# Kernel tuning notes

Measured on AMD Instinct MI355X. Metric: run time of the kernel, lower is better.

Reference implementation:

```python
import jax, jax.numpy as jnp
import numpy as np

B, S, P = 2, 1024, 1024          # batch, new tokens, start_pos (cached prefix)
E, H, KV, HD = 2048, 32, 8, 64    # embed, heads, kv groups, head_dim
G = H // KV                       # group size = 4
THETA = 500000.0
CTX = P + S                       # cache/context length = 2048


def _rope_tables(start, seqlen):
    inv_freq = 1.0 / (THETA ** (jnp.arange(0, HD, 2, dtype=jnp.float32) / HD))
    pos = jnp.arange(start, start + seqlen, dtype=jnp.float32)
    freqs = jnp.outer(pos, inv_freq)              # [S, HD/2]
    emb = jnp.concatenate([freqs, freqs], axis=-1)  # [S, HD]
    return jnp.cos(emb), jnp.sin(emb)


def setup_inputs() -> dict:
    key = jax.random.key(0)
    ks = jax.random.split(key, 8)
    x = jax.random.normal(ks[0], (B, S, E), dtype=jnp.float32)
    cos1, sin1 = _rope_tables(P, S)
    cos = jnp.broadcast_to(cos1[None], (B, S, HD))
    sin = jnp.broadcast_to(sin1[None], (B, S, HD))
    # causal-with-offset additive mask: query i (global pos P+i) sees key j <= P+i
    qpos = P + jnp.arange(S)[:, None]
    kpos = jnp.arange(CTX)[None, :]
    mask = jnp.where(kpos <= qpos, 0.0, -1e9).astype(jnp.float32)[None, None]  # [1,1,S,CTX]
    cache_k = jax.random.normal(ks[1], (B, KV, CTX, HD), dtype=jnp.float32)
    cache_v = jax.random.normal(ks[2], (B, KV, CTX, HD), dtype=jnp.float32)
    sc = 0.02
    Wq = jax.random.normal(ks[3], (E, E), dtype=jnp.float32) * sc
    Wk = jax.random.normal(ks[4], (KV * HD, E), dtype=jnp.float32) * sc
    Wv = jax.random.normal(ks[5], (KV * HD, E), dtype=jnp.float32) * sc
    Wo = jax.random.normal(ks[6], (E, E), dtype=jnp.float32) * sc
    return {"x": x, "cos": cos, "sin": sin, "mask": mask,
            "cache_k": cache_k, "cache_v": cache_v,
            "Wq": Wq, "Wk": Wk, "Wv": Wv, "Wo": Wo, "start_pos": P}


def _rotate_half(t):
    t1, t2 = t[..., : HD // 2], t[..., HD // 2:]
    return jnp.concatenate([-t2, t1], axis=-1)


def _apply_rope(t, cos, sin):
    # t: [B, nh, S, HD]; cos/sin: [B, S, HD] -> unsqueeze head dim
    c = cos[:, None]
    s = sin[:, None]
    return t * c + _rotate_half(t) * s


def reference(x, cos, sin, mask, cache_k, cache_v, Wq, Wk, Wv, Wo, start_pos):
    b, s, e = x.shape
    q = (x @ Wq.T).reshape(b, s, H, HD).transpose(0, 2, 1, 3)    # [B,H,S,HD]
    k = (x @ Wk.T).reshape(b, s, KV, HD).transpose(0, 2, 1, 3)   # [B,KV,S,HD]
    v = (x @ Wv.T).reshape(b, s, KV, HD).transpose(0, 2, 1, 3)
    q = _apply_rope(q, cos, sin)
    k = _apply_rope(k, cos, sin)
    ck = cache_k.at[:, :, start_pos:start_pos + s].set(k)
    cv = cache_v.at[:, :, start_pos:start_pos + s].set(v)
    keys = ck[:, :, : start_pos + s]      # [B,KV,T,HD]
    vals = cv[:, :, : start_pos + s]
    # GQA without materializing repeated KV: view q as [B,KV,G,S,HD]
    qg = q.reshape(b, KV, G, s, HD)
    scores = jnp.einsum("bkgsh,bkth->bkgst", qg, keys) / jnp.sqrt(jnp.float32(HD))
    scores = scores + mask[:, :, None]    # broadcast mask over group dim
    probs = jax.nn.softmax(scores.astype(jnp.float32), axis=-1).astype(x.dtype)
    out = jnp.einsum("bkgst,bkth->bkgsh", probs, vals)            # [B,KV,G,S,HD]
    out = out.reshape(b, H, s, HD).transpose(0, 2, 1, 3).reshape(b, s, e)
    return out @ Wo.T
```

## Files before the change

### kernel.cpp

```cpp
#include <hip/hip_runtime.h>
#include <cstddef>

#define B   2
#define S   1024
#define PP  1024
#define CTX 2048
#define E   2048
#define H   32
#define KVH 8
#define HD  64
#define GQ  4
#define NQKV 3072

typedef short s4v  __attribute__((ext_vector_type(4)));
typedef short s8v  __attribute__((ext_vector_type(8)));
typedef float f4v  __attribute__((ext_vector_type(4)));

__device__ __forceinline__ short f2bf(float f) {
  union { float f; unsigned u; } v; v.f = f;
  unsigned r = v.u + 0x7fffu + ((v.u >> 16) & 1u);
  return (short)(r >> 16);
}
__device__ __forceinline__ float bf2f(short h) {
  union { unsigned u; float f; } v; v.u = ((unsigned)(unsigned short)h) << 16;
  return v.f;
}

__device__ __forceinline__ void gl_lds16(const void* g, void* l) {
  __builtin_amdgcn_global_load_lds((const __attribute__((address_space(1))) unsigned*)g,
                                   (__attribute__((address_space(3))) unsigned*)l, 16, 0, 0);
}

__global__ __launch_bounds__(256) void prep(const float* __restrict__ x,
                                            const float* __restrict__ Wq,
                                            const float* __restrict__ Wk,
                                            const float* __restrict__ Wv,
                                            short* __restrict__ xb,
                                            short* __restrict__ wqkv) {
  const int blk = blockIdx.x, tid = threadIdx.x;
  const float* s; short* d; int base;
  if (blk < 2048)      { s = x;  d = xb;             base = blk; }
  else if (blk < 4096) { s = Wq; d = wqkv;           base = blk - 2048; }
  else if (blk < 4608) { s = Wk; d = wqkv + 4194304; base = blk - 4096; }
  else                 { s = Wv; d = wqkv + 5242880; base = blk - 4608; }
  int i = (base * 256 + tid) * 8;
  float4 a = *(const float4*)&s[i];
  float4 b = *(const float4*)&s[i + 4];
  s8v o;
  o[0]=f2bf(a.x); o[1]=f2bf(a.y); o[2]=f2bf(a.z); o[3]=f2bf(a.w);
  o[4]=f2bf(b.x); o[5]=f2bf(b.y); o[6]=f2bf(b.z); o[7]=f2bf(b.w);
  *(s8v*)&d[i] = o;
}

__global__ __launch_bounds__(256) void qkv_gemm(const short* __restrict__ A,
                                                const short* __restrict__ Bw,
                                                const float* __restrict__ cosb,
                                                const float* __restrict__ sinb,
                                                const float* __restrict__ Wo,
                                                const float* __restrict__ ck,
                                                const float* __restrict__ cv,
                                                short* __restrict__ qb,
                                                short* __restrict__ keys,
                                                short* __restrict__ vt,
                                                short* __restrict__ wob) {
  __shared__ short As[2][8192];
  __shared__ short Bs[2][4096];
  const int tid = threadIdx.x;
  const int id  = blockIdx.x;

  if (id >= 768) {
    const int aux = id - 768;
    if (aux < 2048) {
      int i = (aux * 256 + tid) * 8;
      float4 a = *(const float4*)&Wo[i];
      float4 b = *(const float4*)&Wo[i + 4];
      s8v o;
      o[0]=f2bf(a.x); o[1]=f2bf(a.y); o[2]=f2bf(a.z); o[3]=f2bf(a.w);
      o[4]=f2bf(b.x); o[5]=f2bf(b.y); o[6]=f2bf(b.z); o[7]=f2bf(b.w);
      *(s8v*)&wob[i] = o;
    } else if (aux < 2560) {
      int idx = (aux - 2048) * 256 + tid;
      int bkv = idx >> 13;
      int rem = idx & 8191;
      size_t off = (size_t)bkv * (CTX * HD) + (size_t)rem * 8;
      float4 a = *(const float4*)&ck[off];
      float4 b = *(const float4*)&ck[off + 4];
      s8v o;
      o[0]=f2bf(a.x); o[1]=f2bf(a.y); o[2]=f2bf(a.z); o[3]=f2bf(a.w);
      o[4]=f2bf(b.x); o[5]=f2bf(b.y); o[6]=f2bf(b.z); o[7]=f2bf(b.w);
      *(s8v*)&keys[off] = o;
    } else {
      short (*Ts)[72] = (short (*)[72])&As[0][0];
      const int blk2 = aux - 2560;
      const int bkv = blk2 >> 4;
      const int p0  = (blk2 & 15) * 64;
      const float* src = cv + (size_t)bkv * CTX * HD + (size_t)p0 * HD;
      {
        int dq = tid & 15, kb = tid >> 4;
        float4 vv[4];
#pragma unroll
        for (int i = 0; i < 4; i++)
          vv[i] = *(const float4*)&src[(size_t)(kb * 4 + i) * HD + dq * 4];
#pragma unroll
        for (int j = 0; j < 4; j++) {
          s4v p;
          p[0]=f2bf(((const float*)&vv[0])[j]); p[1]=f2bf(((const float*)&vv[1])[j]);
          p[2]=f2bf(((const float*)&vv[2])[j]); p[3]=f2bf(((const float*)&vv[3])[j]);
          *(s4v*)&Ts[dq * 4 + j][kb * 4] = p;
        }
      }
      __syncthreads();
      {
        int d = tid >> 2, c = tid & 3;
        short* dst = vt + ((size_t)bkv * HD + d) * CTX + p0 + (c >> 1) * 32 + (c & 1) * 4;
#pragma unroll
        for (int j = 0; j < 4; j++) {
          s4v q4 = *(const s4v*)&Ts[d][c * 16 + j * 4];
          *(s4v*)&dst[j * 8] = q4;
        }
      }
    }
    return;
  }

  const int wv   = tid >> 6, lane = tid & 63;
  const int n16  = lane & 15, g = lane >> 4;
  const int m0   = (id / 48) * 128, n0 = (id % 48) * 64;
  const int K = 2048;

  const int rr = tid >> 3;
  const int cc = ((tid & 7) ^ (rr & 7)) * 8;
  const short* pA = A  + (size_t)(m0 + rr) * K + cc;
  const short* pB = Bw + (size_t)(n0 + rr) * K + cc;

  auto stage = [&](int buf, int kofs) {
#pragma unroll
    for (int st = 0; st < 4; st++)
      gl_lds16(pA + kofs + (size_t)st * 32 * K, &As[buf][(st * 256 + wv * 64) * 8]);
#pragma unroll
    for (int st = 0; st < 2; st++)
      gl_lds16(pB + kofs + (size_t)st * 32 * K, &Bs[buf][(st * 256 + wv * 64) * 8]);
  };

  f4v acc[2][4] = {};
  stage(0, 0);
  stage(1, 64);
  int cur = 0;
  for (int k0 = 0; k0 < K; k0 += 64) {
    if (k0 + 64 < K) asm volatile("s_waitcnt vmcnt(6)" ::: "memory");
    else             asm volatile("s_waitcnt vmcnt(0)" ::: "memory");
    __builtin_amdgcn_sched_barrier(0);
    __builtin_amdgcn_s_barrier();

#pragma unroll
    for (int kk = 0; kk < 2; kk++) {
      const int slot = (((kk << 2) | g) ^ (n16 & 7)) * 8;
      s8v af[2], bf[4];
#pragma unroll
      for (int mt = 0; mt < 2; mt++)
        af[mt] = *(const s8v*)&As[cur][(wv * 32 + mt * 16 + n16) * 64 + slot];
#pragma unroll
      for (int nt = 0; nt < 4; nt++)
        bf[nt] = *(const s8v*)&Bs[cur][(nt * 16 + n16) * 64 + slot];
#pragma unroll
      for (int mt = 0; mt < 2; mt++)
#pragma unroll
        for (int nt = 0; nt < 4; nt++)
          acc[mt][nt] = __builtin_amdgcn_mfma_f32_16x16x32_bf16(af[mt], bf[nt], acc[mt][nt], 0, 0, 0);
    }

    __builtin_amdgcn_s_barrier();
    if (k0 + 128 < K) stage(cur, k0 + 128);
    cur ^= 1;
  }

  const int rowb = m0 + wv * 32 + g * 4;
  if (n0 < 2048) {
#pragma unroll
    for (int mt = 0; mt < 2; mt++)
#pragma unroll
      for (int nt = 0; nt < 4; nt++) {
        size_t base = (size_t)(rowb + mt * 16) * E + n0 + nt * 16 + n16;
#pragma unroll
        for (int r = 0; r < 4; r++)
          qb[base + (size_t)r * E] = f2bf(acc[mt][nt][r]);
      }
  } else if (n0 < 2560) {
    const int kvh = (n0 - 2048) >> 6;
#pragma unroll
    for (int mt = 0; mt < 2; mt++) {
      const int row = rowb + mt * 16;
      const int bb = row >> 10, s = row & 1023;
      const float* crow = cosb + ((size_t)bb * S + s) * HD;
      const float* srow = sinb + ((size_t)bb * S + s) * HD;
      const size_t kdst = (((size_t)bb * KVH + kvh) * CTX + PP + s) * HD;
#pragma unroll
      for (int nt = 0; nt < 2; nt++) {
        const int d = n16 + nt * 16;
#pragma unroll
        for (int r = 0; r < 4; r++) {
          float c  = crow[r * HD + d];
          float sn = srow[r * HD + d];
          float k1 = acc[mt][nt][r], k2 = acc[mt][nt + 2][r];
          keys[kdst + (size_t)r * HD + d]      = f2bf(k1 * c - k2 * sn);
          keys[kdst + (size_t)r * HD + d + 32] = f2bf(k2 * c + k1 * sn);
        }
      }
    }
  } else {
    const int b    = m0 >> 10;
    const int head = (n0 - 2560) >> 6;
    const int sbase = (m0 - (b << 10)) + (wv >> 1) * 64;
    const size_t vrowb = (size_t)(b * KVH + head) * HD;
#pragma unroll
    for (int mt = 0; mt < 2; mt++) {
      const int mtp = (wv & 1) * 2 + mt;
      const int pos = PP + sbase + ((mtp >> 1) << 5) + ((mtp & 1) << 2) + (g << 3);
#pragma unroll
      for (int nt = 0; nt < 4; nt++) {
        const int d = nt * 16 + n16;
        s4v o;
        o[0] = f2bf(acc[mt][nt][0]); o[1] = f2bf(acc[mt][nt][1]);
        o[2] = f2bf(acc[mt][nt][2]); o[3] = f2bf(acc[mt][nt][3]);
        *(s4v*)&vt[(vrowb + d) * CTX + pos] = o;
      }
    }
  }
}

__global__ __launch_bounds__(256) void oproj_gemm(const short* __restrict__ A,
                                                  const short* __restrict__ Bw,
                                                  float* __restrict__ C) {
  __shared__ short As[2][8192];
  __shared__ short Bs[2][4096];
  const int tid  = threadIdx.x;
  const int wv   = tid >> 6, lane = tid & 63;
  const int n16  = lane & 15, g = lane >> 4;
  const int id   = blockIdx.x;
  const int m0   = (id >> 5) * 128, n0 = (id & 31) * 64;
  const int K = E, N = E;

  const int rr = tid >> 3;
  const int cc = ((tid & 7) ^ (rr & 7)) * 8;
  const short* pA = A  + (size_t)(m0 + rr) * K + cc;
  const short* pB = Bw + (size_t)(n0 + rr) * K + cc;

  auto stage = [&](int buf, int kofs) {
#pragma unroll
    for (int st = 0; st < 4; st++)
      gl_lds16(pA + kofs + (size_t)st * 32 * K, &As[buf][(st * 256 + wv * 64) * 8]);
#pragma unroll
    for (int st = 0; st < 2; st++)
      gl_lds16(pB + kofs + (size_t)st * 32 * K, &Bs[buf][(st * 256 + wv * 64) * 8]);
  };

  f4v acc[2][4] = {};
  stage(0, 0);
  stage(1, 64);
  int cur = 0;
  for (int k0 = 0; k0 < K; k0 += 64) {
    if (k0 + 64 < K) asm volatile("s_waitcnt vmcnt(6)" ::: "memory");
    else             asm volatile("s_waitcnt vmcnt(0)" ::: "memory");
    __builtin_amdgcn_sched_barrier(0);
    __builtin_amdgcn_s_barrier();

#pragma unroll
    for (int kk = 0; kk < 2; kk++) {
      const int slot = (((kk << 2) | g) ^ (n16 & 7)) * 8;
      s8v af[2], bf[4];
#pragma unroll
      for (int mt = 0; mt < 2; mt++)
        af[mt] = *(const s8v*)&As[cur][(wv * 32 + mt * 16 + n16) * 64 + slot];
#pragma unroll
      for (int nt = 0; nt < 4; nt++)
        bf[nt] = *(const s8v*)&Bs[cur][(nt * 16 + n16) * 64 + slot];
#pragma unroll
      for (int mt = 0; mt < 2; mt++)
#pragma unroll
        for (int nt = 0; nt < 4; nt++)
          acc[mt][nt] = __builtin_amdgcn_mfma_f32_16x16x32_bf16(af[mt], bf[nt], acc[mt][nt], 0, 0, 0);
    }

    __builtin_amdgcn_s_barrier();
    if (k0 + 128 < K) stage(cur, k0 + 128);
    cur ^= 1;
  }

#pragma unroll
  for (int mt = 0; mt < 2; mt++)
#pragma unroll
    for (int nt = 0; nt < 4; nt++) {
      size_t base = (size_t)(m0 + wv * 32 + mt * 16 + g * 4) * N + n0 + nt * 16 + n16;
#pragma unroll
      for (int r = 0; r < 4; r++)
        C[base + (size_t)r * N] = acc[mt][nt][r];
    }
}

__global__ __launch_bounds__(256) void attn_mfma(const short* __restrict__ qb,
                                                 const float* __restrict__ cosb,
                                                 const float* __restrict__ sinb,
                                                 const short* __restrict__ keys,
                                                 const short* __restrict__ valsT,
                                                 short* __restrict__ attn) {
  __shared__ short Ks[4096];
  __shared__ short VTs[4096];

  const int xcd  = blockIdx.x & 7;
  const int j    = blockIdx.x >> 3;
  const int sblk = 15 - (j >> 3);
  const int bkv  = xcd * 2 + ((j >> 2) & 1);
  const int b    = bkv >> 3;
  const int kv   = bkv & 7;
  const int h    = kv * 4 + (j & 3);
  const int sq0  = sblk * 64;
  const int kend = PP + sq0 + 64;

  const int tid  = threadIdx.x;
  const int w    = tid >> 6;
  const int lane = tid & 63;
  const int n    = lane & 15;
  const int g    = lane >> 4;

  const short* kbase = keys  + ((size_t)b * KVH + kv) * CTX * HD;
  const short* vtb   = valsT + ((size_t)b * KVH + kv) * (size_t)HD * CTX;

  union { s4v h4[2]; s8v v; } qlo, qhi;
  {
    const size_t row = (size_t)b * S + sq0 + w * 16 + n;
    const short* qrow = qb + row * E + h * 64;
    const float* crow = cosb + row * HD;
    const float* srow = sinb + row * HD;
    const float SC = 0.18033688011112042f;
    s8v q0 = *(const s8v*)&qrow[g * 8];
    s8v q1 = *(const s8v*)&qrow[32 + g * 8];
    float cc[8], ss[8];
    *(float4*)&cc[0] = *(const float4*)&crow[g * 8];
    *(float4*)&cc[4] = *(const float4*)&crow[g * 8 + 4];
    *(float4*)&ss[0] = *(const float4*)&srow[g * 8];
    *(float4*)&ss[4] = *(const float4*)&srow[g * 8 + 4];
#pragma unroll
    for (int j2 = 0; j2 < 8; j2++) {
      float fl = bf2f(q0[j2]), fh = bf2f(q1[j2]);
      qlo.v[j2] = f2bf((fl * cc[j2] - fh * ss[j2]) * SC);
      qhi.v[j2] = f2bf((fh * cc[j2] + fl * ss[j2]) * SC);
    }
  }

  f4v O[4] = {{0,0,0,0},{0,0,0,0},{0,0,0,0},{0,0,0,0}};
  float la[4] = {0.f, 0.f, 0.f, 0.f};
  const int qp     = PP + sq0 + w * 16 + n;
  const int qmin_w = PP + sq0 + w * 16;

  const int lrow = lane >> 3;
  const int sw   = (lane & 7) ^ lrow;
  const short* kg0 = kbase + (size_t)(w * 8 + lrow) * HD + sw * 8;
  const short* kg1 = kg0 + 32 * HD;
  const short* vg0 = vtb + (size_t)(w * 8 + lrow) * CTX + sw * 8;
  const short* vg1 = vg0 + (size_t)32 * CTX;
  short* kl0 = Ks + w * 512;
  short* kl1 = Ks + 2048 + w * 512;
  short* vl0 = VTs + w * 512;
  short* vl1 = VTs + 2048 + w * 512;

  const int xsl = (g ^ (n & 7)) * 8;

  for (int k0 = 0; k0 < kend; k0 += 64) {
    __syncthreads();
    gl_lds16(kg0 + (size_t)k0 * HD, kl0);
    gl_lds16(kg1 + (size_t)k0 * HD, kl1);
    gl_lds16(vg0 + k0, vl0);
    gl_lds16(vg1 + k0, vl1);
    __syncthreads();

    if (k0 >= qmin_w + 16) continue;

    f4v sc[4];
    __builtin_amdgcn_s_setprio(1);
#pragma unroll
    for (int st = 0; st < 4; st++) {
      const short* krow = &Ks[(st * 16 + n) * 64];
      s8v alo = *(const s8v*)(krow + xsl);
      s8v ahi = *(const s8v*)(krow + (xsl ^ 32));
      f4v z = {0.f, 0.f, 0.f, 0.f};
      z = __builtin_amdgcn_mfma_f32_16x16x32_bf16(alo, qlo.v, z, 0, 0, 0);
      sc[st] = __builtin_amdgcn_mfma_f32_16x16x32_bf16(ahi, qhi.v, z, 0, 0, 0);
    }
    __builtin_amdgcn_s_setprio(0);

    if (k0 + 63 > qmin_w) {
#pragma unroll
      for (int st = 0; st < 4; st++)
#pragma unroll
        for (int r = 0; r < 4; r++) {
          int kpos = k0 + st * 16 + g * 4 + r;
          if (kpos > qp) sc[st][r] = -3e38f;
        }
    }

    union { unsigned u[4]; s8v v; } pb0, pb1;
#pragma unroll
    for (int st = 0; st < 4; st++) {
      float e0 = __builtin_amdgcn_exp2f(sc[st][0]);
      float e1 = __builtin_amdgcn_exp2f(sc[st][1]);
      float e2 = __builtin_amdgcn_exp2f(sc[st][2]);
      float e3 = __builtin_amdgcn_exp2f(sc[st][3]);
      la[0] += e0; la[1] += e1; la[2] += e2; la[3] += e3;
      unsigned w0, w1;
      asm("v_cvt_pk_bf16_f32 %0, %1, %2" : "=v"(w0) : "v"(e0), "v"(e1));
      asm("v_cvt_pk_bf16_f32 %0, %1, %2" : "=v"(w1) : "v"(e2), "v"(e3));
      if (st < 2) { pb0.u[st * 2] = w0; pb0.u[st * 2 + 1] = w1; }
      else        { pb1.u[(st - 2) * 2] = w0; pb1.u[(st - 2) * 2 + 1] = w1; }
    }

    __builtin_amdgcn_s_setprio(1);
#pragma unroll
    for (int dg = 0; dg < 4; dg++) {
      const short* vr = &VTs[(dg * 16 + n) * 64];
      s8v va = *(const s8v*)(vr + xsl);
      s8v vx = *(const s8v*)(vr + (xsl ^ 32));
      O[dg] = __builtin_amdgcn_mfma_f32_16x16x32_bf16(va, pb0.v, O[dg], 0, 0, 0);
      O[dg] = __builtin_amdgcn_mfma_f32_16x16x32_bf16(vx, pb1.v, O[dg], 0, 0, 0);
    }
    __builtin_amdgcn_s_setprio(0);
  }

  float l = (la[0] + la[1]) + (la[2] + la[3]);
  l += __shfl_xor(l, 16);
  l += __shfl_xor(l, 32);
  const float rl = 1.f / l;
  short* orow = attn + ((size_t)b * S + sq0 + w * 16 + n) * E + h * 64;
#pragma unroll
  for (int dg = 0; dg < 4; dg++) {
    s4v o;
    o[0] = f2bf(O[dg][0] * rl); o[1] = f2bf(O[dg][1] * rl);
    o[2] = f2bf(O[dg][2] * rl); o[3] = f2bf(O[dg][3] * rl);
    *(s4v*)&orow[dg * 16 + g * 4] = o;
  }
}

extern "C" void kernel_launch(void* const* d_in, const int* in_sizes, int n_in,
                              void* d_out, int out_size, void* d_ws, size_t ws_size,
                              hipStream_t stream) {
  const float* x       = (const float*)d_in[0];
  const float* cosb    = (const float*)d_in[1];
  const float* sinb    = (const float*)d_in[2];
  const float* cache_k = (const float*)d_in[4];
  const float* cache_v = (const float*)d_in[5];
  const float* Wq      = (const float*)d_in[6];
  const float* Wk      = (const float*)d_in[7];
  const float* Wv      = (const float*)d_in[8];
  const float* Wo      = (const float*)d_in[9];
  float* out = (float*)d_out;

  short* xb    = (short*)d_ws;
  short* wqkv  = xb + 4194304;
  short* wob   = wqkv + 6291456;
  short* keysb = wob + 4194304;
  short* valsT = keysb + 2097152;
  short* aout  = valsT + 2097152;
  short* qb    = aout + 4194304;

  dim3 blk(256);

  prep<<<5120, blk, 0, stream>>>(x, Wq, Wk, Wv, xb, wqkv);

  qkv_gemm<<<3584, blk, 0, stream>>>(xb, wqkv, cosb, sinb, Wo, cache_k, cache_v,
                                     qb, keysb, valsT, wob);

  attn_mfma<<<B * H * (S / 64), blk, 0, stream>>>(qb, cosb, sinb, keysb, valsT, aout);

  oproj_gemm<<<512, blk, 0, stream>>>(aout, wob, out);
}
```

Before: 223.1 us.

## Double-buffer K/V tiles in attention with prefetch two blocks ahead

Splits the K and V^T shared-memory tiles into two buffers. The loads for the block two steps ahead are issued while the current block is computed, and a partial vmcnt wait replaces the two full __syncthreads per iteration. This is meant to hide global-to-LDS load latency behind the MFMA and exp work. It doubles LDS use, which may lower occupancy, and it relies on a hand-counted vmcnt being correct.

```diff
diff --git a/kernel.cpp b/kernel.cpp
--- a/kernel.cpp
+++ b/kernel.cpp
@@ -303,8 +303,8 @@
                                                  const short* __restrict__ keys,
                                                  const short* __restrict__ valsT,
                                                  short* __restrict__ attn) {
-  __shared__ short Ks[4096];
-  __shared__ short VTs[4096];
+  __shared__ short Ks[2][4096];
+  __shared__ short VTs[2][4096];
 
   const int xcd  = blockIdx.x & 7;
   const int j    = blockIdx.x >> 3;
@@ -346,6 +346,7 @@
       qhi.v[j2] = f2bf((fh * cc[j2] + fl * ss[j2]) * SC);
     }
   }
+  __builtin_amdgcn_sched_barrier(0);
 
   f4v O[4] = {{0,0,0,0},{0,0,0,0},{0,0,0,0},{0,0,0,0}};
   float la[4] = {0.f, 0.f, 0.f, 0.f};
@@ -358,71 +359,84 @@
   const short* kg1 = kg0 + 32 * HD;
   const short* vg0 = vtb + (size_t)(w * 8 + lrow) * CTX + sw * 8;
   const short* vg1 = vg0 + (size_t)32 * CTX;
-  short* kl0 = Ks + w * 512;
-  short* kl1 = Ks + 2048 + w * 512;
-  short* vl0 = VTs + w * 512;
-  short* vl1 = VTs + 2048 + w * 512;
+
+  auto stage = [&](int buf, int k0) {
+    short* kl = &Ks[buf][w * 512];
+    short* vl = &VTs[buf][w * 512];
+    gl_lds16(kg0 + (size_t)k0 * HD, kl);
+    gl_lds16(kg1 + (size_t)k0 * HD, kl + 2048);
+    gl_lds16(vg0 + k0, vl);
+    gl_lds16(vg1 + k0, vl + 2048);
+  };
 
   const int xsl = (g ^ (n & 7)) * 8;
 
+  stage(0, 0);
+  stage(1, 64);
+  int cur = 0;
   for (int k0 = 0; k0 < kend; k0 += 64) {
-    __syncthreads();
-    gl_lds16(kg0 + (size_t)k0 * HD, kl0);
-    gl_lds16(kg1 + (size_t)k0 * HD, kl1);
-    gl_lds16(vg0 + k0, vl0);
-    gl_lds16(vg1 + k0, vl1);
-    __syncthreads();
-
-    if (k0 >= qmin_w + 16) continue;
-
-    f4v sc[4];
-    __builtin_amdgcn_s_setprio(1);
-#pragma unroll
-    for (int st = 0; st < 4; st++) {
-      const short* krow = &Ks[(st * 16 + n) * 64];
-      s8v alo = *(const s8v*)(krow + xsl);
-      s8v ahi = *(const s8v*)(krow + (xsl ^ 32));
-      f4v z = {0.f, 0.f, 0.f, 0.f};
-      z = __builtin_amdgcn_mfma_f32_16x16x32_bf16(alo, qlo.v, z, 0, 0, 0);
-      sc[st] = __builtin_amdgcn_mfma_f32_16x16x32_bf16(ahi, qhi.v, z, 0, 0, 0);
-    }
-    __builtin_amdgcn_s_setprio(0);
-
-    if (k0 + 63 > qmin_w) {
-#pragma unroll
-      for (int st = 0; st < 4; st++)
-#pragma unroll
-        for (int r = 0; r < 4; r++) {
-          int kpos = k0 + st * 16 + g * 4 + r;
-          if (kpos > qp) sc[st][r] = -3e38f;
-        }
-    }
-
-    union { unsigned u[4]; s8v v; } pb0, pb1;
-#pragma unroll
-    for (int st = 0; st < 4; st++) {
-      float e0 = __builtin_amdgcn_exp2f(sc[st][0]);
-      float e1 = __builtin_amdgcn_exp2f(sc[st][1]);
-      float e2 = __builtin_amdgcn_exp2f(sc[st][2]);
-      float e3 = __builtin_amdgcn_exp2f(sc[st][3]);
-      la[0] += e0; la[1] += e1; la[2] += e2; la[3] += e3;
-      unsigned w0, w1;
-      asm("v_cvt_pk_bf16_f32 %0, %1, %2" : "=v"(w0) : "v"(e0), "v"(e1));
-      asm("v_cvt_pk_bf16_f32 %0, %1, %2" : "=v"(w1) : "v"(e2), "v"(e3));
-      if (st < 2) { pb0.u[st * 2] = w0; pb0.u[st * 2 + 1] = w1; }
-      else        { pb1.u[(st - 2) * 2] = w0; pb1.u[(st - 2) * 2 + 1] = w1; }
-    }
-
-    __builtin_amdgcn_s_setprio(1);
-#pragma unroll
-    for (int dg = 0; dg < 4; dg++) {
-      const short* vr = &VTs[(dg * 16 + n) * 64];
-      s8v va = *(const s8v*)(vr + xsl);
-      s8v vx = *(const s8v*)(vr + (xsl ^ 32));
-      O[dg] = __builtin_amdgcn_mfma_f32_16x16x32_bf16(va, pb0.v, O[dg], 0, 0, 0);
-      O[dg] = __builtin_amdgcn_mfma_f32_16x16x32_bf16(vx, pb1.v, O[dg], 0, 0, 0);
-    }
-    __builtin_amdgcn_s_setprio(0);
+    if (k0 + 64 < kend) asm volatile("s_waitcnt vmcnt(4)" ::: "memory");
+    else                asm volatile("s_waitcnt vmcnt(0)" ::: "memory");
+    __builtin_amdgcn_sched_barrier(0);
+    __builtin_amdgcn_s_barrier();
+
+    if (k0 < qmin_w + 16) {
+      const short* kb = &Ks[cur][0];
+      const short* vb = &VTs[cur][0];
+
+      f4v sc[4];
+      __builtin_amdgcn_s_setprio(1);
+#pragma unroll
+      for (int st = 0; st < 4; st++) {
+        const short* krow = kb + (st * 16 + n) * 64;
+        s8v alo = *(const s8v*)(krow + xsl);
+        s8v ahi = *(const s8v*)(krow + (xsl ^ 32));
+        f4v z = {0.f, 0.f, 0.f, 0.f};
+        z = __builtin_amdgcn_mfma_f32_16x16x32_bf16(alo, qlo.v, z, 0, 0, 0);
+        sc[st] = __builtin_amdgcn_mfma_f32_16x16x32_bf16(ahi, qhi.v, z, 0, 0, 0);
+      }
+      __builtin_amdgcn_s_setprio(0);
+
+      if (k0 + 63 > qmin_w) {
+#pragma unroll
+        for (int st = 0; st < 4; st++)
+#pragma unroll
+          for (int r = 0; r < 4; r++) {
+            int kpos = k0 + st * 16 + g * 4 + r;
+            if (kpos > qp) sc[st][r] = -3e38f;
+          }
+      }
+
+      union { unsigned u[4]; s8v v; } pb0, pb1;
+#pragma unroll
+      for (int st = 0; st < 4; st++) {
+        float e0 = __builtin_amdgcn_exp2f(sc[st][0]);
+        float e1 = __builtin_amdgcn_exp2f(sc[st][1]);
+        float e2 = __builtin_amdgcn_exp2f(sc[st][2]);
+        float e3 = __builtin_amdgcn_exp2f(sc[st][3]);
+        la[0] += e0; la[1] += e1; la[2] += e2; la[3] += e3;
+        unsigned w0, w1;
+        asm("v_cvt_pk_bf16_f32 %0, %1, %2" : "=v"(w0) : "v"(e0), "v"(e1));
+        asm("v_cvt_pk_bf16_f32 %0, %1, %2" : "=v"(w1) : "v"(e2), "v"(e3));
+        if (st < 2) { pb0.u[st * 2] = w0; pb0.u[st * 2 + 1] = w1; }
+        else        { pb1.u[(st - 2) * 2] = w0; pb1.u[(st - 2) * 2 + 1] = w1; }
+      }
+
+      __builtin_amdgcn_s_setprio(1);
+#pragma unroll
+      for (int dg = 0; dg < 4; dg++) {
+        const short* vr = vb + (dg * 16 + n) * 64;
+        s8v va = *(const s8v*)(vr + xsl);
+        s8v vx = *(const s8v*)(vr + (xsl ^ 32));
+        O[dg] = __builtin_amdgcn_mfma_f32_16x16x32_bf16(va, pb0.v, O[dg], 0, 0, 0);
+        O[dg] = __builtin_amdgcn_mfma_f32_16x16x32_bf16(vx, pb1.v, O[dg], 0, 0, 0);
+      }
+      __builtin_amdgcn_s_setprio(0);
+    }
+
+    __builtin_amdgcn_s_barrier();
+    if (k0 + 128 < kend) stage(cur, k0 + 128);
+    cur ^= 1;
   }
 
   float l = (la[0] + la[1]) + (la[2] + la[3]);
```

Result: no change. 226.0 us (+1.3%).
